# Kernel optimization log

Hardware: AMD Instinct MI355X
Metric: run time of the kernel (lower is better)

Reference implementation:

```python
import jax, jax.numpy as jnp
import numpy as np
from jax import lax

B, CIN, H, W = 8, 256, 64, 64
CC = 128          # corr_channels
COUT = 64         # out_channels
KH = KW = 5       # corr_kernel_size
SH = SW = 1       # corr_stride
PT, PB = KH // 2, (KH + 1) // 2 - 1   # pad='k'
PL, PR = KW // 2, (KW + 1) // 2 - 1


def setup_inputs() -> dict:
    key = jax.random.key(0)
    k1, k2, k3, k4, k5 = jax.random.split(key, 5)
    x = jax.random.normal(k1, (B, CIN, H, W), dtype=jnp.float32)
    w_ext = jax.random.normal(k2, (CC, CIN, 3, 3), dtype=jnp.float32) * 0.02
    b_ext = jax.random.normal(k3, (CC,), dtype=jnp.float32) * 0.02
    w_reg = jax.random.normal(k4, (COUT, CC, KH, KW), dtype=jnp.float32) * 0.02
    b_reg = jax.random.normal(k5, (COUT,), dtype=jnp.float32) * 0.02
    return {"x": x, "w_ext": w_ext, "b_ext": b_ext, "w_reg": w_reg, "b_reg": b_reg}


def _forward(x, w_ext, b_ext, w_reg, b_reg):
    # feature extraction: 3x3 conv, padding 1
    f = lax.conv_general_dilated(x, w_ext, (1, 1), ((1, 1), (1, 1)))
    f = f + b_ext[None, :, None, None]
    # local autocorrelation: multiply each window element by the window center, per channel
    fp = jnp.pad(f, ((0, 0), (0, 0), (PT, PB), (PL, PR)))
    nH = (fp.shape[2] - KH) // SH + 1
    nW = (fp.shape[3] - KW) // SW + 1
    center = fp[:, :, KH // 2:KH // 2 + nH * SH:SH, KW // 2:KW // 2 + nW * SW:SW]  # [B,CC,nH,nW]
    patches = jnp.stack(
        [fp[:, :, u:u + nH * SH:SH, v:v + nW * SW:SW] for u in range(KH) for v in range(KW)],
        axis=-1)  # [B,CC,nH,nW,KH*KW]
    corr = patches * center[..., None]  # [B,CC,nH,nW,KH*KW]
    out = jnp.einsum('bcijk,ock->bijo', corr, w_reg.reshape(COUT, CC, KH * KW))
    out = out + b_reg
    return out.transpose(0, 3, 1, 2)  # permute=True -> [B, COUT, nH, nW]


def reference(x, w_ext, b_ext, w_reg, b_reg):
    return _forward(x, w_ext, b_ext, w_reg, b_reg)
```

## Files before the change

### kernel.cpp

```cpp
#include <hip/hip_runtime.h>
#include <hip/hip_bf16.h>

#define B_    8
#define CIN_  256
#define CC_   128
#define COUT_ 64
#define HP_   68
#define HPX_  (HP_ * HP_)
#define XQW_  66
#define XQPX_ (XQW_ * XQW_)

typedef __attribute__((ext_vector_type(8))) short bh8;
typedef __attribute__((ext_vector_type(4))) float f4;

__device__ __forceinline__ ushort f2bf(float f) {
    uint u = __float_as_uint(f);
    return (ushort)((u + 0x7fffu + ((u >> 16) & 1u)) >> 16);
}
__device__ __forceinline__ float bf2f(ushort s) {
    return __uint_as_float(((uint)s) << 16);
}
__device__ __forceinline__ short f2bf_c(float f) {
    __hip_bfloat16 h = __float2bfloat16(f);
    short s;
    __builtin_memcpy(&s, &h, 2);
    return s;
}

#define NB_MISC 2217
__global__ __launch_bounds__(256) void prep_all(const float* __restrict__ x,
                                                const float* __restrict__ w_ext,
                                                const float* __restrict__ w_reg,
                                                short* __restrict__ wg,
                                                short* __restrict__ wa,
                                                ushort* __restrict__ fpad_t,
                                                ushort* __restrict__ xq) {
    __shared__ float xt[2][32][65];
    const int tid = threadIdx.x;
    if (blockIdx.x < NB_MISC) {
        int e = blockIdx.x * 256 + tid;
        if (e < 67584) {
            int seg = e & 15;
            int t = e >> 4;
            int b = t / 528, rp = t - b * 528;
            int i, j;
            if (rp < 136) { i = rp / 68; j = rp - (rp / 68) * 68; }
            else if (rp < 272) { int r = rp - 136; i = 66 + r / 68; j = r - (r / 68) * 68; }
            else { int r = rp - 272; i = 2 + (r >> 2); int c = r & 3; j = (c < 2) ? c : c + 64; }
            uint4 z; z.x = 0u; z.y = 0u; z.z = 0u; z.w = 0u;
            *(uint4*)&fpad_t[(((size_t)b * HPX_) + i * HP_ + j) * 128 + seg * 8] = z;
            return;
        }
        e -= 67584;
        if (e < 294912) {
            int ci = e & 31;
            int t  = e >> 5;
            int cc = t & 127;
            int t2 = t >> 7;
            int rs = t2 % 9, cb = t2 / 9;
            wg[e] = (short)f2bf(w_ext[(cc * CIN_ + cb * 32 + ci) * 9 + rs]);
            return;
        }
        e -= 294912;
        if (e < 204800) {
            int ci = e & 31;
            int o  = (e >> 5) & 63;
            int rest = e >> 11;
            int k = rest % 25, q = rest / 25;
            wa[e] = (short)f2bf(w_reg[(o * CC_ + q * 32 + ci) * 25 + k]);
        }
        return;
    }

    const int pid = blockIdx.x - NB_MISC;
    const int rp = pid % 33, cb = (pid / 33) & 7, b = pid / 264;

#pragma unroll
    for (int rr = 0; rr < 2; ++rr) {
        int y = rp * 2 + rr - 1;
        if ((unsigned)y < 64u) {
            int xx = tid & 63, wv = tid >> 6;
#pragma unroll
            for (int it = 0; it < 8; ++it) {
                int ci = it * 4 + wv;
                xt[rr][ci][xx] = x[(((size_t)(b * CIN_ + cb * 32 + ci)) * 64 + y) * 64 + xx];
            }
        }
    }
    __syncthreads();

    for (int e = tid; e < 528; e += 256) {
        int rr = e / 264, t = e - rr * 264;
        int hc = t >> 2, seg = t & 3;
        int y = rp * 2 + rr - 1, xx = hc - 1;
        uint pk[4] = {0u, 0u, 0u, 0u};
        if ((unsigned)y < 64u && (unsigned)xx < 64u) {
#pragma unroll
            for (int i = 0; i < 4; ++i) {
                uint lo = f2bf(xt[rr][seg * 8 + i * 2][xx]);
                uint hi = f2bf(xt[rr][seg * 8 + i * 2 + 1][xx]);
                pk[i] = lo | (hi << 16);
            }
        }
        uint4 v; v.x = pk[0]; v.y = pk[1]; v.z = pk[2]; v.w = pk[3];
        *(uint4*)&xq[((((size_t)(b * 8 + cb)) * XQPX_) + (rp * 2 + rr) * XQW_ + hc) * 32 + seg * 8] = v;
    }
}

__global__ __launch_bounds__(256)
__attribute__((amdgpu_waves_per_eu(2, 2)))
void conv3x3_mfma(const ushort* __restrict__ xq,
                  const short* __restrict__ wg,
                  const float* __restrict__ bext,
                  ushort* __restrict__ fpad_t) {
    __shared__ __align__(16) short xh[2][100 * 72];
    __shared__ __align__(16) short wlds[2][3 * 128 * 32];
    const int tid = threadIdx.x;
    const int lane = tid & 63, wv = tid >> 6;
    const int j0 = blockIdx.x * 8, i0 = blockIdx.y * 8, b = blockIdx.z;
    const int l15 = lane & 15, kg = lane >> 4;
    const int cc0 = wv * 32;

    int abase[2];
#pragma unroll
    for (int mm = 0; mm < 2; ++mm) {
        int cc = cc0 + mm * 16 + l15;
        abase[mm] = cc * 32 + ((((cc >> 1) + kg) & 3) << 3);
    }
    int xb[4];
#pragma unroll
    for (int nn = 0; nn < 4; ++nn) {
        int px = nn * 16 + l15, pi = px >> 3, pj = px & 7;
        xb[nn] = (pi * 10 + pj) * 72 + kg * 8;
    }
    int wdst[6]; int goff[6];
#pragma unroll
    for (int k = 0; k < 6; ++k) {
        int c = tid + k * 256;
        int cc = (c & 511) >> 2, kgc = c & 3;
        wdst[k] = (c >> 9) * 4096 + cc * 32 + ((((cc >> 1) + kgc) & 3) << 3);
        goff[k] = c * 8;
    }
    const int hp0 = tid >> 2, seg0 = tid & 3;
    const int hr0 = hp0 / 10, hc0 = hp0 - hr0 * 10;
    const int xsrc0 = ((i0 + hr0) * XQW_ + (j0 + hc0)) * 32 + seg0 * 8;
    const int xdst0 = hp0 * 72 + seg0 * 8;
    const int hp1 = (tid + 256) >> 2;
    const int hr1 = hp1 / 10, hc1 = hp1 - hr1 * 10;
    const int xsrc1 = ((i0 + hr1) * XQW_ + (j0 + hc1)) * 32 + seg0 * 8;
    const int xdst1 = hp1 * 72 + seg0 * 8;
    const bool x1ok = tid < 144;

    f4 acc[2][4] = {};

    {
#pragma unroll
        for (int k = 0; k < 6; ++k)
            *(bh8*)&wlds[0][wdst[k]] = *(const bh8*)(wg + goff[k]);
        const ushort* xbase = xq + (((size_t)(b * 8 + 0)) * XQPX_) * 32;
        *(bh8*)&xh[0][xdst0] = *(const bh8*)&xbase[xsrc0];
        if (x1ok) *(bh8*)&xh[0][xdst1] = *(const bh8*)&xbase[xsrc1];
    }
    __syncthreads();

    int p = 0;
#pragma unroll 1
    for (int cb = 0; cb < 8; ++cb) {
        const int xbuf = cb & 1;
#pragma unroll 1
        for (int g = 0; g < 3; ++g) {
            const int buf = p & 1;
            const bool wmore = (p < 23);
            const bool xmore = (g == 2) && (cb < 7);

            bh8 wreg[6];
            const short* gsrc = wg + (size_t)(wmore ? (p + 1) : 23) * 12288;
#pragma unroll
            for (int k = 0; k < 6; ++k)
                wreg[k] = *(const bh8*)(gsrc + goff[k]);
            bh8 xr0, xr1;
            if (xmore) {
                const ushort* xbase = xq + (((size_t)(b * 8 + cb + 1)) * XQPX_) * 32;
                xr0 = *(const bh8*)&xbase[xsrc0];
                if (x1ok) xr1 = *(const bh8*)&xbase[xsrc1];
            }

            const short* wb = wlds[buf];
            const int goffs = g * 10 * 72;
#pragma unroll
            for (int s = 0; s < 3; ++s) {
                bh8 a[2], bb[4];
#pragma unroll
                for (int mm = 0; mm < 2; ++mm)
                    a[mm] = *(const bh8*)&wb[s * 4096 + abase[mm]];
#pragma unroll
                for (int nn = 0; nn < 4; ++nn)
                    bb[nn] = *(const bh8*)&xh[xbuf][xb[nn] + goffs + s * 72];
#pragma unroll
                for (int mm = 0; mm < 2; ++mm)
#pragma unroll
                    for (int nn = 0; nn < 4; ++nn)
                        acc[mm][nn] = __builtin_amdgcn_mfma_f32_16x16x32_bf16(
                            a[mm], bb[nn], acc[mm][nn], 0, 0, 0);
            }

            if (wmore) {
#pragma unroll
                for (int k = 0; k < 6; ++k)
                    *(bh8*)&wlds[buf ^ 1][wdst[k]] = wreg[k];
            }
            if (xmore) {
                *(bh8*)&xh[xbuf ^ 1][xdst0] = xr0;
                if (x1ok) *(bh8*)&xh[xbuf ^ 1][xdst1] = xr1;
            }
            __syncthreads();
            ++p;
        }
    }

#pragma unroll
    for (int mm = 0; mm < 2; ++mm) {
        const int ccb = cc0 + mm * 16 + kg * 4;
        float bv0 = bext[ccb + 0], bv1 = bext[ccb + 1];
        float bv2 = bext[ccb + 2], bv3 = bext[ccb + 3];
#pragma unroll
        for (int nn = 0; nn < 4; ++nn) {
            int px = nn * 16 + l15, pi = px >> 3, pj = px & 7;
            size_t row = (size_t)b * HPX_ + (2 + i0 + pi) * HP_ + (2 + j0 + pj);
            uint lo = (uint)f2bf(acc[mm][nn][0] + bv0) | ((uint)f2bf(acc[mm][nn][1] + bv1) << 16);
            uint hi = (uint)f2bf(acc[mm][nn][2] + bv2) | ((uint)f2bf(acc[mm][nn][3] + bv3) << 16);
            uint2 pk; pk.x = lo; pk.y = hi;
            *(uint2*)&fpad_t[row * 128 + ccb] = pk;
        }
    }
}

__global__ __launch_bounds__(512)
__attribute__((amdgpu_waves_per_eu(2, 2)))
void autocorr_mfma(const ushort* __restrict__ ft,
                   const short* __restrict__ wA,
                   const float* __restrict__ breg,
                   float* __restrict__ out) {
    __shared__ __align__(16) short flds[240 * 136];
    __shared__ __align__(16) short wlds[2][5 * 64 * 32];
    const int tid = threadIdx.x;
    const int lane = tid & 63, wv = tid >> 6;
    const int oh = wv >> 2, pxg = wv & 3;
    const int j0 = blockIdx.x * 16, i0 = blockIdx.y * 8, b = blockIdx.z;
    const int l15 = lane & 15, kg = lane >> 4;

    int abase[2];
#pragma unroll
    for (int mm = 0; mm < 2; ++mm) {
        int o = oh * 32 + mm * 16 + l15;
        abase[mm] = o * 32 + ((((o >> 1) + kg) & 3) << 3);
    }
    int wdst[3]; int goff[3];
#pragma unroll
    for (int k = 0; k < 3; ++k) {
        int c = tid + k * 512;
        int o = (c & 255) >> 2, kgc = c & 3;
        wdst[k] = (c >> 8) * 2048 + o * 32 + ((((o >> 1) + kgc) & 3) << 3);
        goff[k] = c * 8;
    }
    const bool w3 = tid < 256;

    for (int e = tid; e < 3840; e += 512) {
        int hp = e >> 4, seg = e & 15;
        int hr = hp / 20, hc = hp - hr * 20;
        const ushort* src = ft + ((size_t)b * HPX_ + (i0 + hr) * HP_ + (j0 + hc)) * 128 + seg * 8;
        *(bh8*)&flds[hp * 136 + seg * 8] = *(const bh8*)src;
    }
    *(bh8*)&wlds[0][wdst[0]] = *(const bh8*)(wA + goff[0]);
    *(bh8*)&wlds[0][wdst[1]] = *(const bh8*)(wA + goff[1]);
    if (w3) *(bh8*)&wlds[0][wdst[2]] = *(const bh8*)(wA + goff[2]);
    __syncthreads();

    f4 acc[2][2] = {};
    int base_off[2], cen_off[2];
#pragma unroll
    for (int t = 0; t < 2; ++t) {
        int px = pxg * 32 + t * 16 + l15;
        int pi = px >> 4, pj = px & 15;
        base_off[t] = (pi * 20 + pj) * 136 + kg * 8;
        cen_off[t]  = ((pi + 2) * 20 + (pj + 2)) * 136 + kg * 8;
    }

    int p = 0;
#pragma unroll 1
    for (int q = 0; q < 4; ++q) {
        float cen[2][8];
#pragma unroll
        for (int t = 0; t < 2; ++t) {
            bh8 c8 = *(const bh8*)&flds[cen_off[t] + q * 32];
#pragma unroll
            for (int jj = 0; jj < 8; ++jj) cen[t][jj] = bf2f((ushort)c8[jj]);
        }
#pragma unroll 1
        for (int u = 0; u < 5; ++u) {
            const int buf = p & 1;
            const bool wmore = (p < 19);

            bh8 wreg0, wreg1, wreg2;
            const short* gsrc = wA + (size_t)(wmore ? (p + 1) : 19) * 10240;
            wreg0 = *(const bh8*)(gsrc + goff[0]);
            wreg1 = *(const bh8*)(gsrc + goff[1]);
            if (w3) wreg2 = *(const bh8*)(gsrc + goff[2]);

            const short* wb = wlds[buf];
#pragma unroll
            for (int v = 0; v < 5; ++v) {
                const int koff = (u * 20 + v) * 136;
                bh8 a[2];
#pragma unroll
                for (int mm = 0; mm < 2; ++mm)
                    a[mm] = *(const bh8*)&wb[v * 2048 + abase[mm]];
                bh8 bb[2];
#pragma unroll
                for (int t = 0; t < 2; ++t) {
                    bh8 s8 = *(const bh8*)&flds[base_off[t] + q * 32 + koff];
#pragma unroll
                    for (int jj = 0; jj < 8; ++jj) {
                        float pr = bf2f((ushort)s8[jj]) * cen[t][jj];
                        bb[t][jj] = f2bf_c(pr);
                    }
                }
#pragma unroll
                for (int mm = 0; mm < 2; ++mm)
#pragma unroll
                    for (int t = 0; t < 2; ++t)
                        acc[mm][t] = __builtin_amdgcn_mfma_f32_16x16x32_bf16(
                            a[mm], bb[t], acc[mm][t], 0, 0, 0);
            }

            if (wmore) {
                *(bh8*)&wlds[buf ^ 1][wdst[0]] = wreg0;
                *(bh8*)&wlds[buf ^ 1][wdst[1]] = wreg1;
                if (w3) *(bh8*)&wlds[buf ^ 1][wdst[2]] = wreg2;
            }
            __syncthreads();
            ++p;
        }
    }

#pragma unroll
    for (int mm = 0; mm < 2; ++mm) {
#pragma unroll
        for (int reg = 0; reg < 4; ++reg) {
            int o = oh * 32 + mm * 16 + kg * 4 + reg;
            float bv = breg[o];
#pragma unroll
            for (int t = 0; t < 2; ++t) {
                int px = pxg * 32 + t * 16 + l15, pi = px >> 4, pj = px & 15;
                out[(((size_t)(b * COUT_ + o)) * 64 + i0 + pi) * 64 + j0 + pj] =
                    acc[mm][t][reg] + bv;
            }
        }
    }
}

extern "C" void kernel_launch(void* const* d_in, const int* in_sizes, int n_in,
                              void* d_out, int out_size, void* d_ws, size_t ws_size,
                              hipStream_t stream) {
    const float* x     = (const float*)d_in[0];
    const float* w_ext = (const float*)d_in[1];
    const float* b_ext = (const float*)d_in[2];
    const float* w_reg = (const float*)d_in[3];
    const float* b_reg = (const float*)d_in[4];
    float* out = (float*)d_out;

    char* ws = (char*)d_ws;
    const size_t FPADT_BYTES = (size_t)B_ * HPX_ * 128 * 2;
    const size_t WG_BYTES    = (size_t)8 * 9 * 128 * 32 * 2;
    const size_t WA_BYTES    = (size_t)4 * 25 * 64 * 32 * 2;
    ushort* fpad_t = (ushort*)ws;
    short*  wgq    = (short*)(ws + FPADT_BYTES);
    short*  wa     = (short*)(ws + FPADT_BYTES + WG_BYTES);
    ushort* xq     = (ushort*)(ws + FPADT_BYTES + WG_BYTES + WA_BYTES);

    prep_all<<<NB_MISC + 33 * 8 * 8, 256, 0, stream>>>(x, w_ext, w_reg, wgq, wa, fpad_t, xq);

    dim3 cgrid(8, 8, 8);
    conv3x3_mfma<<<cgrid, 256, 0, stream>>>(xq, wgq, b_ext, fpad_t);
    dim3 agrid(4, 8, 8);
    autocorr_mfma<<<agrid, 512, 0, stream>>>(fpad_t, wa, b_reg, out);
}
```

Before: 74.29 us.

## Enlarge conv tiles and split autocorr channels across blocks with atomic accumulation

The conv3x3 kernel now uses 512-thread blocks covering 8x16 pixel tiles, so each block loads a weight slice once for twice the pixels. The autocorr kernel now tiles 16x16 pixels with all 64 outputs per wave and splits the 128 correlation channels into two halves across blocks. The halves are summed into the output with atomic adds, so prep_all now zeroes the output and only the first half adds the bias. This aims to cut redundant weight and feature reloads and raise per-block MFMA reuse, at the cost of an extra output-zeroing pass and atomic traffic.

```diff
diff --git a/kernel.cpp b/kernel.cpp
--- a/kernel.cpp
+++ b/kernel.cpp
@@ -27,14 +27,15 @@
     return s;
 }
 
-#define NB_MISC 2217
+#define NB_MISC 4264
 __global__ __launch_bounds__(256) void prep_all(const float* __restrict__ x,
                                                 const float* __restrict__ w_ext,
                                                 const float* __restrict__ w_reg,
                                                 short* __restrict__ wg,
                                                 short* __restrict__ wa,
                                                 ushort* __restrict__ fpad_t,
-                                                ushort* __restrict__ xq) {
+                                                ushort* __restrict__ xq,
+                                                float* __restrict__ out) {
     __shared__ float xt[2][32][65];
     const int tid = threadIdx.x;
     if (blockIdx.x < NB_MISC) {
@@ -68,6 +69,12 @@
             int rest = e >> 11;
             int k = rest % 25, q = rest / 25;
             wa[e] = (short)f2bf(w_reg[(o * CC_ + q * 32 + ci) * 25 + k]);
+            return;
+        }
+        e -= 204800;
+        if (e < 524288) {
+            float4 z; z.x = 0.f; z.y = 0.f; z.z = 0.f; z.w = 0.f;
+            *(float4*)&out[(size_t)e * 4] = z;
         }
         return;
     }
@@ -107,19 +114,20 @@
     }
 }
 
-__global__ __launch_bounds__(256)
+__global__ __launch_bounds__(512)
 __attribute__((amdgpu_waves_per_eu(2, 2)))
 void conv3x3_mfma(const ushort* __restrict__ xq,
                   const short* __restrict__ wg,
                   const float* __restrict__ bext,
                   ushort* __restrict__ fpad_t) {
-    __shared__ __align__(16) short xh[2][100 * 72];
+    __shared__ __align__(16) short xh[2][180 * 72];
     __shared__ __align__(16) short wlds[2][3 * 128 * 32];
     const int tid = threadIdx.x;
     const int lane = tid & 63, wv = tid >> 6;
-    const int j0 = blockIdx.x * 8, i0 = blockIdx.y * 8, b = blockIdx.z;
+    const int ch = wv >> 1, pg = wv & 1;
+    const int j0 = blockIdx.x * 16, i0 = blockIdx.y * 8, b = blockIdx.z;
     const int l15 = lane & 15, kg = lane >> 4;
-    const int cc0 = wv * 32;
+    const int cc0 = ch * 32;
 
     int abase[2];
 #pragma unroll
@@ -130,36 +138,37 @@
     int xb[4];
 #pragma unroll
     for (int nn = 0; nn < 4; ++nn) {
-        int px = nn * 16 + l15, pi = px >> 3, pj = px & 7;
-        xb[nn] = (pi * 10 + pj) * 72 + kg * 8;
-    }
-    int wdst[6]; int goff[6];
-#pragma unroll
-    for (int k = 0; k < 6; ++k) {
-        int c = tid + k * 256;
+        int px = pg * 64 + nn * 16 + l15, pi = px >> 4, pj = px & 15;
+        xb[nn] = (pi * 18 + pj) * 72 + kg * 8;
+    }
+    int wdst[3]; int goff[3];
+#pragma unroll
+    for (int k = 0; k < 3; ++k) {
+        int c = tid + k * 512;
         int cc = (c & 511) >> 2, kgc = c & 3;
         wdst[k] = (c >> 9) * 4096 + cc * 32 + ((((cc >> 1) + kgc) & 3) << 3);
         goff[k] = c * 8;
     }
-    const int hp0 = tid >> 2, seg0 = tid & 3;
-    const int hr0 = hp0 / 10, hc0 = hp0 - hr0 * 10;
-    const int xsrc0 = ((i0 + hr0) * XQW_ + (j0 + hc0)) * 32 + seg0 * 8;
-    const int xdst0 = hp0 * 72 + seg0 * 8;
-    const int hp1 = (tid + 256) >> 2;
-    const int hr1 = hp1 / 10, hc1 = hp1 - hr1 * 10;
-    const int xsrc1 = ((i0 + hr1) * XQW_ + (j0 + hc1)) * 32 + seg0 * 8;
-    const int xdst1 = hp1 * 72 + seg0 * 8;
-    const bool x1ok = tid < 144;
+    int xsrc[2], xdst[2];
+#pragma unroll
+    for (int k = 0; k < 2; ++k) {
+        int c = tid + k * 512;
+        int hp = c >> 2, seg = c & 3;
+        int hr = hp / 18, hc = hp - hr * 18;
+        xsrc[k] = ((i0 + hr) * XQW_ + (j0 + hc)) * 32 + seg * 8;
+        xdst[k] = hp * 72 + seg * 8;
+    }
+    const bool x1ok = tid < 208;
 
     f4 acc[2][4] = {};
 
     {
 #pragma unroll
-        for (int k = 0; k < 6; ++k)
+        for (int k = 0; k < 3; ++k)
             *(bh8*)&wlds[0][wdst[k]] = *(const bh8*)(wg + goff[k]);
         const ushort* xbase = xq + (((size_t)(b * 8 + 0)) * XQPX_) * 32;
-        *(bh8*)&xh[0][xdst0] = *(const bh8*)&xbase[xsrc0];
-        if (x1ok) *(bh8*)&xh[0][xdst1] = *(const bh8*)&xbase[xsrc1];
+        *(bh8*)&xh[0][xdst[0]] = *(const bh8*)&xbase[xsrc[0]];
+        if (x1ok) *(bh8*)&xh[0][xdst[1]] = *(const bh8*)&xbase[xsrc[1]];
     }
     __syncthreads();
 
@@ -173,20 +182,19 @@
             const bool wmore = (p < 23);
             const bool xmore = (g == 2) && (cb < 7);
 
-            bh8 wreg[6];
+            bh8 wreg[3];
             const short* gsrc = wg + (size_t)(wmore ? (p + 1) : 23) * 12288;
 #pragma unroll
-            for (int k = 0; k < 6; ++k)
+            for (int k = 0; k < 3; ++k)
                 wreg[k] = *(const bh8*)(gsrc + goff[k]);
             bh8 xr0, xr1;
             if (xmore) {
                 const ushort* xbase = xq + (((size_t)(b * 8 + cb + 1)) * XQPX_) * 32;
-                xr0 = *(const bh8*)&xbase[xsrc0];
-                if (x1ok) xr1 = *(const bh8*)&xbase[xsrc1];
+                xr0 = *(const bh8*)&xbase[xsrc[0]];
+                if (x1ok) xr1 = *(const bh8*)&xbase[xsrc[1]];
             }
 
             const short* wb = wlds[buf];
-            const int goffs = g * 10 * 72;
 #pragma unroll
             for (int s = 0; s < 3; ++s) {
                 bh8 a[2], bb[4];
@@ -195,7 +203,7 @@
                     a[mm] = *(const bh8*)&wb[s * 4096 + abase[mm]];
 #pragma unroll
                 for (int nn = 0; nn < 4; ++nn)
-                    bb[nn] = *(const bh8*)&xh[xbuf][xb[nn] + goffs + s * 72];
+                    bb[nn] = *(const bh8*)&xh[xbuf][xb[nn] + (g * 18 + s) * 72];
 #pragma unroll
                 for (int mm = 0; mm < 2; ++mm)
 #pragma unroll
@@ -206,12 +214,12 @@
 
             if (wmore) {
 #pragma unroll
-                for (int k = 0; k < 6; ++k)
+                for (int k = 0; k < 3; ++k)
                     *(bh8*)&wlds[buf ^ 1][wdst[k]] = wreg[k];
             }
             if (xmore) {
-                *(bh8*)&xh[xbuf ^ 1][xdst0] = xr0;
-                if (x1ok) *(bh8*)&xh[xbuf ^ 1][xdst1] = xr1;
+                *(bh8*)&xh[xbuf ^ 1][xdst[0]] = xr0;
+                if (x1ok) *(bh8*)&xh[xbuf ^ 1][xdst[1]] = xr1;
             }
             __syncthreads();
             ++p;
@@ -225,7 +233,7 @@
         float bv2 = bext[ccb + 2], bv3 = bext[ccb + 3];
 #pragma unroll
         for (int nn = 0; nn < 4; ++nn) {
-            int px = nn * 16 + l15, pi = px >> 3, pj = px & 7;
+            int px = pg * 64 + nn * 16 + l15, pi = px >> 4, pj = px & 15;
             size_t row = (size_t)b * HPX_ + (2 + i0 + pi) * HP_ + (2 + j0 + pj);
             uint lo = (uint)f2bf(acc[mm][nn][0] + bv0) | ((uint)f2bf(acc[mm][nn][1] + bv1) << 16);
             uint hi = (uint)f2bf(acc[mm][nn][2] + bv2) | ((uint)f2bf(acc[mm][nn][3] + bv3) << 16);
@@ -241,18 +249,18 @@
                    const short* __restrict__ wA,
                    const float* __restrict__ breg,
                    float* __restrict__ out) {
-    __shared__ __align__(16) short flds[240 * 136];
+    __shared__ __align__(16) short flds[400 * 72];
     __shared__ __align__(16) short wlds[2][5 * 64 * 32];
     const int tid = threadIdx.x;
     const int lane = tid & 63, wv = tid >> 6;
-    const int oh = wv >> 2, pxg = wv & 3;
-    const int j0 = blockIdx.x * 16, i0 = blockIdx.y * 8, b = blockIdx.z;
+    const int j0 = blockIdx.x * 16, i0 = blockIdx.y * 16;
+    const int b = blockIdx.z >> 1, h = blockIdx.z & 1;
     const int l15 = lane & 15, kg = lane >> 4;
 
-    int abase[2];
-#pragma unroll
-    for (int mm = 0; mm < 2; ++mm) {
-        int o = oh * 32 + mm * 16 + l15;
+    int abase[4];
+#pragma unroll
+    for (int mm = 0; mm < 4; ++mm) {
+        int o = mm * 16 + l15;
         abase[mm] = o * 32 + ((((o >> 1) + kg) & 3) << 3);
     }
     int wdst[3]; int goff[3];
@@ -264,45 +272,46 @@
         goff[k] = c * 8;
     }
     const bool w3 = tid < 256;
-
-    for (int e = tid; e < 3840; e += 512) {
-        int hp = e >> 4, seg = e & 15;
+    const short* wbase_g = wA + (size_t)h * 102400;
+
+    for (int e = tid; e < 3200; e += 512) {
+        int hp = e >> 3, seg = e & 7;
         int hr = hp / 20, hc = hp - hr * 20;
-        const ushort* src = ft + ((size_t)b * HPX_ + (i0 + hr) * HP_ + (j0 + hc)) * 128 + seg * 8;
-        *(bh8*)&flds[hp * 136 + seg * 8] = *(const bh8*)src;
-    }
-    *(bh8*)&wlds[0][wdst[0]] = *(const bh8*)(wA + goff[0]);
-    *(bh8*)&wlds[0][wdst[1]] = *(const bh8*)(wA + goff[1]);
-    if (w3) *(bh8*)&wlds[0][wdst[2]] = *(const bh8*)(wA + goff[2]);
+        const ushort* src = ft + ((size_t)b * HPX_ + (i0 + hr) * HP_ + (j0 + hc)) * 128 + (h * 8 + seg) * 8;
+        *(bh8*)&flds[hp * 72 + seg * 8] = *(const bh8*)src;
+    }
+    *(bh8*)&wlds[0][wdst[0]] = *(const bh8*)(wbase_g + goff[0]);
+    *(bh8*)&wlds[0][wdst[1]] = *(const bh8*)(wbase_g + goff[1]);
+    if (w3) *(bh8*)&wlds[0][wdst[2]] = *(const bh8*)(wbase_g + goff[2]);
     __syncthreads();
 
-    f4 acc[2][2] = {};
+    f4 acc[4][2] = {};
     int base_off[2], cen_off[2];
 #pragma unroll
     for (int t = 0; t < 2; ++t) {
-        int px = pxg * 32 + t * 16 + l15;
+        int px = wv * 32 + t * 16 + l15;
         int pi = px >> 4, pj = px & 15;
-        base_off[t] = (pi * 20 + pj) * 136 + kg * 8;
-        cen_off[t]  = ((pi + 2) * 20 + (pj + 2)) * 136 + kg * 8;
+        base_off[t] = (pi * 20 + pj) * 72 + kg * 8;
+        cen_off[t]  = ((pi + 2) * 20 + (pj + 2)) * 72 + kg * 8;
     }
 
     int p = 0;
 #pragma unroll 1
-    for (int q = 0; q < 4; ++q) {
+    for (int qq = 0; qq < 2; ++qq) {
         float cen[2][8];
 #pragma unroll
         for (int t = 0; t < 2; ++t) {
-            bh8 c8 = *(const bh8*)&flds[cen_off[t] + q * 32];
+            bh8 c8 = *(const bh8*)&flds[cen_off[t] + qq * 32];
 #pragma unroll
             for (int jj = 0; jj < 8; ++jj) cen[t][jj] = bf2f((ushort)c8[jj]);
         }
 #pragma unroll 1
         for (int u = 0; u < 5; ++u) {
             const int buf = p & 1;
-            const bool wmore = (p < 19);
+            const bool wmore = (p < 9);
 
             bh8 wreg0, wreg1, wreg2;
-            const short* gsrc = wA + (size_t)(wmore ? (p + 1) : 19) * 10240;
+            const short* gsrc = wbase_g + (size_t)(wmore ? (p + 1) : 9) * 10240;
             wreg0 = *(const bh8*)(gsrc + goff[0]);
             wreg1 = *(const bh8*)(gsrc + goff[1]);
             if (w3) wreg2 = *(const bh8*)(gsrc + goff[2]);
@@ -310,15 +319,15 @@
             const short* wb = wlds[buf];
 #pragma unroll
             for (int v = 0; v < 5; ++v) {
-                const int koff = (u * 20 + v) * 136;
-                bh8 a[2];
-#pragma unroll
-                for (int mm = 0; mm < 2; ++mm)
+                const int koff = (u * 20 + v) * 72;
+                bh8 a[4];
+#pragma unroll
+                for (int mm = 0; mm < 4; ++mm)
                     a[mm] = *(const bh8*)&wb[v * 2048 + abase[mm]];
                 bh8 bb[2];
 #pragma unroll
                 for (int t = 0; t < 2; ++t) {
-                    bh8 s8 = *(const bh8*)&flds[base_off[t] + q * 32 + koff];
+                    bh8 s8 = *(const bh8*)&flds[base_off[t] + qq * 32 + koff];
 #pragma unroll
                     for (int jj = 0; jj < 8; ++jj) {
                         float pr = bf2f((ushort)s8[jj]) * cen[t][jj];
@@ -326,7 +335,7 @@
                     }
                 }
 #pragma unroll
-                for (int mm = 0; mm < 2; ++mm)
+                for (int mm = 0; mm < 4; ++mm)
 #pragma unroll
                     for (int t = 0; t < 2; ++t)
                         acc[mm][t] = __builtin_amdgcn_mfma_f32_16x16x32_bf16(
@@ -344,16 +353,17 @@
     }
 
 #pragma unroll
-    for (int mm = 0; mm < 2; ++mm) {
+    for (int mm = 0; mm < 4; ++mm) {
 #pragma unroll
         for (int reg = 0; reg < 4; ++reg) {
-            int o = oh * 32 + mm * 16 + kg * 4 + reg;
-            float bv = breg[o];
+            int o = mm * 16 + kg * 4 + reg;
+            float bv = (h == 0) ? breg[o] : 0.f;
 #pragma unroll
             for (int t = 0; t < 2; ++t) {
-                int px = pxg * 32 + t * 16 + l15, pi = px >> 4, pj = px & 15;
-                out[(((size_t)(b * COUT_ + o)) * 64 + i0 + pi) * 64 + j0 + pj] =
-                    acc[mm][t][reg] + bv;
+                int px = wv * 32 + t * 16 + l15, pi = px >> 4, pj = px & 15;
+                float* dst = &out[(((size_t)(b * COUT_ + o)) * 64 + i0 + pi) * 64 + j0 + pj];
+                __hip_atomic_fetch_add(dst, acc[mm][t][reg] + bv,
+                                       __ATOMIC_RELAXED, __HIP_MEMORY_SCOPE_AGENT);
             }
         }
     }
@@ -378,10 +388,10 @@
     short*  wa     = (short*)(ws + FPADT_BYTES + WG_BYTES);
     ushort* xq     = (ushort*)(ws + FPADT_BYTES + WG_BYTES + WA_BYTES);
 
-    prep_all<<<NB_MISC + 33 * 8 * 8, 256, 0, stream>>>(x, w_ext, w_reg, wgq, wa, fpad_t, xq);
-
-    dim3 cgrid(8, 8, 8);
-    conv3x3_mfma<<<cgrid, 256, 0, stream>>>(xq, wgq, b_ext, fpad_t);
-    dim3 agrid(4, 8, 8);
+    prep_all<<<NB_MISC + 33 * 8 * 8, 256, 0, stream>>>(x, w_ext, w_reg, wgq, wa, fpad_t, xq, out);
+
+    dim3 cgrid(4, 8, 8);
+    conv3x3_mfma<<<cgrid, 512, 0, stream>>>(xq, wgq, b_ext, fpad_t);
+    dim3 agrid(4, 4, 16);
     autocorr_mfma<<<agrid, 512, 0, stream>>>(fpad_t, wa, b_reg, out);
 }
```

Result: no change. 74.41 us (+0.2%).
